# Kernel tuning notes

Measured on AMD Instinct MI355X. Metric: run time of the kernel, lower is better.

The kernel has to match this reference:

```python
import jax, jax.numpy as jnp
import numpy as np

N_NODES = 100_000
N_EDGES = 1_600_000
F_IN, H, C = 128, 128, 64


def setup_inputs() -> dict:
    key = jax.random.key(0)
    ks = jax.random.split(key, 12)
    s = 0.05  # weight init scale
    features = jax.random.normal(ks[0], (N_NODES, F_IN), jnp.float32)
    src = jax.random.randint(ks[1], (N_EDGES,), 0, N_NODES)
    dst = jax.random.randint(ks[2], (N_EDGES,), 0, N_NODES)
    return {
        "features": features,
        "src": src,
        "dst": dst,
        "Ws0": jax.random.normal(ks[3], (F_IN, H), jnp.float32) * s,
        "Wn0": jax.random.normal(ks[4], (F_IN, H), jnp.float32) * s,
        "b0": jnp.zeros((H,), jnp.float32),
        "Ws1": jax.random.normal(ks[5], (H, H), jnp.float32) * s,
        "Wn1": jax.random.normal(ks[6], (H, H), jnp.float32) * s,
        "b1": jnp.zeros((H,), jnp.float32),
        "Ws2": jax.random.normal(ks[7], (H, C), jnp.float32) * s,
        "Wn2": jax.random.normal(ks[8], (H, C), jnp.float32) * s,
        "b2": jnp.zeros((C,), jnp.float32),
    }


def sage_conv(feat, src, dst, Ws, Wn, b):
    """DGL SAGEConv with mean aggregator: fc_self(h) + fc_neigh(mean_{u->v} h_u) + b."""
    n = feat.shape[0]
    deg = jax.ops.segment_sum(jnp.ones(src.shape[0], feat.dtype), dst, num_segments=n)
    # gather src features along edges, reduce by dst (irregular gather-scatter)
    neigh = jax.ops.segment_sum(feat[src], dst, num_segments=n)
    neigh = neigh / jnp.maximum(deg, 1.0)[:, None]
    return feat @ Ws + neigh @ Wn + b


def reference(features, src, dst, Ws0, Wn0, b0, Ws1, Wn1, b1, Ws2, Wn2, b2):
    # eval mode: dropout is identity
    h = sage_conv(features, src, dst, Ws0, Wn0, b0)
    h = jax.nn.relu(h)
    h = sage_conv(h, src, dst, Ws1, Wn1, b1)
    h = jax.nn.relu(h)
    h = sage_conv(h, src, dst, Ws2, Wn2, b2)
    return h
```

## Files before the change

kernel.cpp:

```cpp
#include <hip/hip_runtime.h>

typedef _Float16 f16x8 __attribute__((ext_vector_type(8)));
typedef _Float16 f16x4 __attribute__((ext_vector_type(4)));
typedef _Float16 f16x2 __attribute__((ext_vector_type(2)));
typedef float f32x4 __attribute__((ext_vector_type(4)));


#define BSHIFT 7
#define BSZ 128
#define EPB 16384

__global__ __launch_bounds__(256) void histA(const int* __restrict__ dst,
                                             int* __restrict__ hist_pb,
                                             int n_edges, int nbk) {
  __shared__ unsigned lh[1024];
  for (int i = threadIdx.x; i < nbk; i += 256) lh[i] = 0;
  __syncthreads();
  int base = blockIdx.x * EPB;
  for (int i = threadIdx.x; i < EPB; i += 256) {
    int e = base + i;
    if (e < n_edges) atomicAdd(&lh[dst[e] >> BSHIFT], 1u);
  }
  __syncthreads();
  for (int i = threadIdx.x; i < nbk; i += 256)
    hist_pb[(size_t)blockIdx.x * nbk + i] = (int)lh[i];
}

__global__ __launch_bounds__(256) void sumB1(const int* __restrict__ hist_pb,
                                             int* __restrict__ btot, int nblk, int nbk) {
  int b = blockIdx.x * 256 + threadIdx.x;
  if (b >= nbk) return;
  int s = 0;
  for (int k = 0; k < nblk; ++k) s += hist_pb[(size_t)k * nbk + b];
  btot[b] = s;
}

__global__ __launch_bounds__(1024) void scanB2(const int* __restrict__ btot,
                                               int* __restrict__ bbase, int nbk) {
  __shared__ int buf[1024];
  int t = threadIdx.x;
  int v = (t < nbk) ? btot[t] : 0;
  int x = v;
  buf[t] = x;
  __syncthreads();
#pragma unroll
  for (int off = 1; off < 1024; off <<= 1) {
    int tm = (t >= off) ? buf[t - off] : 0;
    __syncthreads();
    x += tm;
    buf[t] = x;
    __syncthreads();
  }
  if (t < nbk) bbase[t] = x - v;
  if (t == nbk - 1) bbase[nbk] = x;
}

__global__ __launch_bounds__(256) void offsB3(int* __restrict__ hist_pb,
                                              const int* __restrict__ bbase,
                                              int nblk, int nbk) {
  int b = blockIdx.x * 256 + threadIdx.x;
  if (b >= nbk) return;
  int run = bbase[b];
  for (int k = 0; k < nblk; ++k) {
    int t = hist_pb[(size_t)k * nbk + b];
    hist_pb[(size_t)k * nbk + b] = run;
    run += t;
  }
}

__global__ __launch_bounds__(256) void scatC(const int* __restrict__ src,
                                             const int* __restrict__ dst,
                                             const int* __restrict__ hist_pb,
                                             unsigned* __restrict__ pairs,
                                             int n_edges, int nbk) {
  __shared__ unsigned lofs[1024];
  for (int i = threadIdx.x; i < nbk; i += 256)
    lofs[i] = (unsigned)hist_pb[(size_t)blockIdx.x * nbk + i];
  __syncthreads();
  int base = blockIdx.x * EPB;
  for (int i = threadIdx.x; i < EPB; i += 256) {
    int e = base + i;
    if (e < n_edges) {
      int d = dst[e];
      unsigned pos = atomicAdd(&lofs[d >> BSHIFT], 1u);
      pairs[pos] = ((unsigned)(d & (BSZ - 1)) << 18) | (unsigned)src[e];
    }
  }
}

__global__ __launch_bounds__(256) void finalD(const unsigned* __restrict__ pairs,
                                              const int* __restrict__ bbase,
                                              int* __restrict__ deg,
                                              int* __restrict__ row_ptr,
                                              int* __restrict__ src_sorted,
                                              int n, int nbk) {
  __shared__ int ldeg[BSZ];
  __shared__ int lscan[BSZ];
  __shared__ int lcur[BSZ];
  int b = blockIdx.x;
  int t = threadIdx.x;
  int node0 = b << BSHIFT;
  int beg = bbase[b], end = bbase[b + 1];
  if (t < BSZ) ldeg[t] = 0;
  __syncthreads();
  for (int i = beg + t; i < end; i += 256) atomicAdd(&ldeg[pairs[i] >> 18], 1);
  __syncthreads();
  int x = (t < BSZ) ? ldeg[t] : 0;
  if (t < BSZ) lscan[t] = x;
  __syncthreads();
#pragma unroll
  for (int off = 1; off < BSZ; off <<= 1) {
    int tm = (t >= off && t < BSZ) ? lscan[t - off] : 0;
    __syncthreads();
    if (t < BSZ) {
      x += tm;
      lscan[t] = x;
    }
    __syncthreads();
  }
  if (t < BSZ) {
    int node = node0 + t;
    lcur[t] = beg + lscan[t] - ldeg[t];
    if (node < n) {
      deg[node] = ldeg[t];
      row_ptr[node + 1] = beg + lscan[t];
      if (node == 0) row_ptr[0] = 0;
    }
  }
  __syncthreads();
  for (int i = beg + t; i < end; i += 256) {
    unsigned p = pairs[i];
    int pos = atomicAdd(&lcur[p >> 18], 1);
    src_sorted[pos] = (int)(p & 0x3FFFFu);
  }
}

__global__ __launch_bounds__(256) void convert_features(const float* __restrict__ f,
                                                        _Float16* __restrict__ X, int n) {
  int idx = blockIdx.x * 256 + threadIdx.x;
  int total = n * 32;
  if (idx >= total) return;
  int node = idx >> 5;
  int c4 = (idx & 31) * 4;
  float4 v = *(const float4*)(f + (size_t)node * 128 + c4);
  _Float16* o = X + (size_t)node * 256 + c4;
  o[0] = (_Float16)v.x;
  o[1] = (_Float16)v.y;
  o[2] = (_Float16)v.z;
  o[3] = (_Float16)v.w;
}

__global__ __launch_bounds__(256) void build_wt(const float* __restrict__ Ws,
                                                const float* __restrict__ Wn,
                                                _Float16* __restrict__ Wt, int NOUT) {
  int idx = blockIdx.x * 256 + threadIdx.x;
  if (idx >= NOUT * 256) return;
  int nn = idx >> 8;
  int k = idx & 255;
  float v = (k < 128) ? Ws[(size_t)k * NOUT + nn] : Wn[(size_t)(k - 128) * NOUT + nn];
  Wt[(size_t)nn * 256 + k] = (_Float16)v;
}

__global__ __launch_bounds__(256) void aggregate_f16(
    const _Float16* __restrict__ X, const int* __restrict__ row_ptr,
    const int* __restrict__ src_sorted, const int* __restrict__ deg,
    _Float16* __restrict__ Xout, int n) {
  int gid = blockIdx.x * 256 + threadIdx.x;
  int node = gid >> 6;
  if (node >= n) return;
  int lane = threadIdx.x & 63;
  int fh = lane & 31;
  int es = lane >> 5;
  int beg = row_ptr[node];
  int end = row_ptr[node + 1];
  float a0 = 0.f, a1 = 0.f, a2 = 0.f, a3 = 0.f;
  int e = beg;
  for (; e + 8 <= end; e += 8) {
    int s0 = src_sorted[e + 0 + es];
    int s1 = src_sorted[e + 2 + es];
    int s2 = src_sorted[e + 4 + es];
    int s3 = src_sorted[e + 6 + es];
    f16x4 v0 = *(const f16x4*)(X + (size_t)s0 * 256 + fh * 4);
    f16x4 v1 = *(const f16x4*)(X + (size_t)s1 * 256 + fh * 4);
    f16x4 v2 = *(const f16x4*)(X + (size_t)s2 * 256 + fh * 4);
    f16x4 v3 = *(const f16x4*)(X + (size_t)s3 * 256 + fh * 4);
    a0 += (float)v0[0] + (float)v1[0] + (float)v2[0] + (float)v3[0];
    a1 += (float)v0[1] + (float)v1[1] + (float)v2[1] + (float)v3[1];
    a2 += (float)v0[2] + (float)v1[2] + (float)v2[2] + (float)v3[2];
    a3 += (float)v0[3] + (float)v1[3] + (float)v2[3] + (float)v3[3];
  }
  for (; e < end; e += 2) {
    if (e + es < end) {
      int s = src_sorted[e + es];
      f16x4 v = *(const f16x4*)(X + (size_t)s * 256 + fh * 4);
      a0 += (float)v[0];
      a1 += (float)v[1];
      a2 += (float)v[2];
      a3 += (float)v[3];
    }
  }
  a0 += __shfl_xor(a0, 32);
  a1 += __shfl_xor(a1, 32);
  a2 += __shfl_xor(a2, 32);
  a3 += __shfl_xor(a3, 32);
  if (es == 0) {
    float inv = 1.0f / fmaxf((float)(end - beg), 1.0f);
    f16x4 o;
    o[0] = (_Float16)(a0 * inv);
    o[1] = (_Float16)(a1 * inv);
    o[2] = (_Float16)(a2 * inv);
    o[3] = (_Float16)(a3 * inv);
    *(f16x4*)(Xout + (size_t)node * 256 + 128 + fh * 4) = o;
  }
}

template <int NOUT, bool RELU, bool FINAL>
__global__ __launch_bounds__(256) void gemm_mfma(
    const _Float16* __restrict__ X, const _Float16* __restrict__ Wt,
    const float* __restrict__ bias, _Float16* __restrict__ outX,
    float* __restrict__ outF, int n) {
  constexpr int CW = NOUT / 2;
  constexpr int CF = CW / 16;
  __shared__ _Float16 Xs[128][72];
  __shared__ _Float16 Wc[NOUT][72];

  int tid = threadIdx.x;
  int lane = tid & 63;
  int wid = tid >> 6;
  int wr = wid >> 1;
  int wc = wid & 1;
  int node0 = blockIdx.x * 128;

  f32x4 acc[4][CF];
#pragma unroll
  for (int i = 0; i < 4; ++i)
#pragma unroll
    for (int j = 0; j < CF; ++j) acc[i][j] = {0.f, 0.f, 0.f, 0.f};

#pragma unroll
  for (int c = 0; c < 4; ++c) {
    int k0 = c * 64;
#pragma unroll
    for (int i = 0; i < 4; ++i) {
      int idx = i * 256 + tid;
      int r = idx >> 3;
      int o = (idx & 7) * 8;
      f16x8 v;
#pragma unroll
      for (int z = 0; z < 8; ++z) v[z] = (_Float16)0.f;
      int node = node0 + r;
      if (node < n) v = *(const f16x8*)(X + (size_t)node * 256 + k0 + o);
      *(f16x8*)&Xs[r][o] = v;
    }
#pragma unroll
    for (int i = 0; i < NOUT / 32; ++i) {
      int idx = i * 256 + tid;
      int r = idx >> 3;
      int o = (idx & 7) * 8;
      *(f16x8*)&Wc[r][o] = *(const f16x8*)(Wt + (size_t)r * 256 + k0 + o);
    }
    __syncthreads();
#pragma unroll
    for (int ks = 0; ks < 2; ++ks) {
      int kk = ks * 32 + (lane >> 4) * 8;
      f16x8 a[4], b[CF];
#pragma unroll
      for (int i = 0; i < 4; ++i)
        a[i] = *(const f16x8*)&Xs[wr * 64 + i * 16 + (lane & 15)][kk];
#pragma unroll
      for (int j = 0; j < CF; ++j)
        b[j] = *(const f16x8*)&Wc[wc * CW + j * 16 + (lane & 15)][kk];
#pragma unroll
      for (int i = 0; i < 4; ++i)
#pragma unroll
        for (int j = 0; j < CF; ++j)
          acc[i][j] = __builtin_amdgcn_mfma_f32_16x16x32_f16(a[i], b[j], acc[i][j], 0, 0, 0);
    }
    __syncthreads();
  }

#pragma unroll
  for (int j = 0; j < CF; ++j) {
    int col = wc * CW + j * 16 + (lane & 15);
    float bv = bias[col];
#pragma unroll
    for (int i = 0; i < 4; ++i) {
#pragma unroll
      for (int q = 0; q < 4; ++q) {
        int row = wr * 64 + i * 16 + (lane >> 4) * 4 + q;
        int node = node0 + row;
        if (node < n) {
          float v = acc[i][j][q] + bv;
          if (RELU) v = fmaxf(v, 0.f);
          if (FINAL)
            outF[(size_t)node * NOUT + col] = v;
          else
            outX[(size_t)node * 256 + col] = (_Float16)v;
        }
      }
    }
  }
}

extern "C" void kernel_launch(void* const* d_in, const int* in_sizes, int n_in,
                              void* d_out, int out_size, void* d_ws, size_t ws_size,
                              hipStream_t stream) {
  const float* features = (const float*)d_in[0];
  const int* src = (const int*)d_in[1];
  const int* dst = (const int*)d_in[2];
  const float* Ws0 = (const float*)d_in[3];
  const float* Wn0 = (const float*)d_in[4];
  const float* b0 = (const float*)d_in[5];
  const float* Ws1 = (const float*)d_in[6];
  const float* Wn1 = (const float*)d_in[7];
  const float* b1 = (const float*)d_in[8];
  const float* Ws2 = (const float*)d_in[9];
  const float* Wn2 = (const float*)d_in[10];
  const float* b2 = (const float*)d_in[11];

  const int n = in_sizes[0] / 128;
  const int n_edges = in_sizes[1];
  const int nbk = (n + BSZ - 1) >> BSHIFT;
  const int nblk = (n_edges + EPB - 1) / EPB;

  char* ws = (char*)d_ws;
  size_t off = 0;
  auto alloc = [&](size_t bytes) -> void* {
    void* p = ws + off;
    off += (bytes + 255) & ~(size_t)255;
    return p;
  };
  int* hist_pb = (int*)alloc((size_t)nblk * nbk * 4);
  int* btot = (int*)alloc((size_t)nbk * 4);
  int* bbase = (int*)alloc(((size_t)nbk + 1) * 4);
  unsigned* pairs = (unsigned*)alloc((size_t)n_edges * 4);
  int* deg = (int*)alloc((size_t)n * 4);
  int* row_ptr = (int*)alloc(((size_t)n + 1) * 4);
  int* src_sorted = (int*)alloc((size_t)n_edges * 4);
  _Float16* XA = (_Float16*)alloc((size_t)n * 256 * 2);
  _Float16* XB = (_Float16*)alloc((size_t)n * 256 * 2);
  _Float16* Wt0 = (_Float16*)alloc((size_t)128 * 256 * 2);
  _Float16* Wt1 = (_Float16*)alloc((size_t)128 * 256 * 2);
  _Float16* Wt2 = (_Float16*)alloc((size_t)64 * 256 * 2);

  int nbkb = (nbk + 255) / 256;
  histA<<<nblk, 256, 0, stream>>>(dst, hist_pb, n_edges, nbk);
  sumB1<<<nbkb, 256, 0, stream>>>(hist_pb, btot, nblk, nbk);
  scanB2<<<1, 1024, 0, stream>>>(btot, bbase, nbk);
  offsB3<<<nbkb, 256, 0, stream>>>(hist_pb, bbase, nblk, nbk);
  scatC<<<nblk, 256, 0, stream>>>(src, dst, hist_pb, pairs, n_edges, nbk);
  finalD<<<nbk, 256, 0, stream>>>(pairs, bbase, deg, row_ptr, src_sorted, n, nbk);

  convert_features<<<(n * 32 + 255) / 256, 256, 0, stream>>>(features, XA, n);
  build_wt<<<(128 * 256 + 255) / 256, 256, 0, stream>>>(Ws0, Wn0, Wt0, 128);
  build_wt<<<(128 * 256 + 255) / 256, 256, 0, stream>>>(Ws1, Wn1, Wt1, 128);
  build_wt<<<(64 * 256 + 255) / 256, 256, 0, stream>>>(Ws2, Wn2, Wt2, 64);

  int agg_blocks = (int)(((size_t)n * 64 + 255) / 256);
  int gemm_blocks = (n + 127) / 128;

  aggregate_f16<<<agg_blocks, 256, 0, stream>>>(XA, row_ptr, src_sorted, deg, XA, n);
  gemm_mfma<128, true, false><<<gemm_blocks, 256, 0, stream>>>(XA, Wt0, b0, XB, nullptr, n);
  aggregate_f16<<<agg_blocks, 256, 0, stream>>>(XB, row_ptr, src_sorted, deg, XB, n);
  gemm_mfma<128, true, false><<<gemm_blocks, 256, 0, stream>>>(XB, Wt1, b1, XA, nullptr, n);
  aggregate_f16<<<agg_blocks, 256, 0, stream>>>(XA, row_ptr, src_sorted, deg, XA, n);
  gemm_mfma<64, false, true><<<gemm_blocks, 256, 0, stream>>>(XA, Wt2, b2, nullptr, (float*)d_out, n);
}
```

Baseline: 538.4 us.

## Reorder final layer to transform before aggregating, shrink sort blocks, use fma_mix accumulation

The last SAGE layer now computes both linear projections first: one GEMM writes the self term plus bias into the output and the neighbour projection (64 wide, fp16) into a scratch buffer. A new 64-wide aggregation kernel then adds the neighbour mean, so the final gather reads 64 features per edge instead of 128. Separately, the edge-bucketing kernels use smaller edge chunks with a block-to-chunk remap to spread work across XCDs, and the aggregation inner loops use v_fma_mix to accumulate fp16 into fp32 without separate converts. The unused degree array is dropped. Costs: an extra kernel launch, a read-modify-write of the fp32 output, and a larger per-chunk histogram array to sum and scan.

```diff
diff --git a/kernel.cpp b/kernel.cpp
--- a/kernel.cpp
+++ b/kernel.cpp
@@ -2,28 +2,43 @@
 
 typedef _Float16 f16x8 __attribute__((ext_vector_type(8)));
 typedef _Float16 f16x4 __attribute__((ext_vector_type(4)));
-typedef _Float16 f16x2 __attribute__((ext_vector_type(2)));
 typedef float f32x4 __attribute__((ext_vector_type(4)));
 
 
 #define BSHIFT 7
 #define BSZ 128
-#define EPB 16384
+#define EPB 2048
+
+__device__ __forceinline__ int work_of_block(int b, int nblk) {
+  int q = nblk >> 3, r = nblk & 7;
+  int x = b & 7, i = b >> 3;
+  return (x < r) ? x * (q + 1) + i : r * (q + 1) + (x - r) * q + i;
+}
+
+__device__ __forceinline__ void mixlo(float& a, unsigned v) {
+  asm("v_fma_mix_f32 %0, %1, 1.0, %0 op_sel:[0,0,0] op_sel_hi:[1,0,0]"
+      : "+v"(a) : "v"(v));
+}
+__device__ __forceinline__ void mixhi(float& a, unsigned v) {
+  asm("v_fma_mix_f32 %0, %1, 1.0, %0 op_sel:[1,0,0] op_sel_hi:[1,0,0]"
+      : "+v"(a) : "v"(v));
+}
 
 __global__ __launch_bounds__(256) void histA(const int* __restrict__ dst,
                                              int* __restrict__ hist_pb,
-                                             int n_edges, int nbk) {
+                                             int n_edges, int nbk, int nblk) {
   __shared__ unsigned lh[1024];
   for (int i = threadIdx.x; i < nbk; i += 256) lh[i] = 0;
   __syncthreads();
-  int base = blockIdx.x * EPB;
+  int w = work_of_block(blockIdx.x, nblk);
+  int base = w * EPB;
   for (int i = threadIdx.x; i < EPB; i += 256) {
     int e = base + i;
     if (e < n_edges) atomicAdd(&lh[dst[e] >> BSHIFT], 1u);
   }
   __syncthreads();
   for (int i = threadIdx.x; i < nbk; i += 256)
-    hist_pb[(size_t)blockIdx.x * nbk + i] = (int)lh[i];
+    hist_pb[(size_t)w * nbk + i] = (int)lh[i];
 }
 
 __global__ __launch_bounds__(256) void sumB1(const int* __restrict__ hist_pb,
@@ -72,12 +87,13 @@
                                              const int* __restrict__ dst,
                                              const int* __restrict__ hist_pb,
                                              unsigned* __restrict__ pairs,
-                                             int n_edges, int nbk) {
+                                             int n_edges, int nbk, int nblk) {
   __shared__ unsigned lofs[1024];
+  int w = work_of_block(blockIdx.x, nblk);
   for (int i = threadIdx.x; i < nbk; i += 256)
-    lofs[i] = (unsigned)hist_pb[(size_t)blockIdx.x * nbk + i];
-  __syncthreads();
-  int base = blockIdx.x * EPB;
+    lofs[i] = (unsigned)hist_pb[(size_t)w * nbk + i];
+  __syncthreads();
+  int base = w * EPB;
   for (int i = threadIdx.x; i < EPB; i += 256) {
     int e = base + i;
     if (e < n_edges) {
@@ -90,7 +106,6 @@
 
 __global__ __launch_bounds__(256) void finalD(const unsigned* __restrict__ pairs,
                                               const int* __restrict__ bbase,
-                                              int* __restrict__ deg,
                                               int* __restrict__ row_ptr,
                                               int* __restrict__ src_sorted,
                                               int n, int nbk) {
@@ -122,7 +137,6 @@
     int node = node0 + t;
     lcur[t] = beg + lscan[t] - ldeg[t];
     if (node < n) {
-      deg[node] = ldeg[t];
       row_ptr[node + 1] = beg + lscan[t];
       if (node == 0) row_ptr[0] = 0;
     }
@@ -161,10 +175,20 @@
   Wt[(size_t)nn * 256 + k] = (_Float16)v;
 }
 
+__global__ __launch_bounds__(256) void build_wt2cat(const float* __restrict__ Ws2,
+                                                    const float* __restrict__ Wn2,
+                                                    _Float16* __restrict__ Wt) {
+  int idx = blockIdx.x * 256 + threadIdx.x;
+  if (idx >= 128 * 128) return;
+  int nn = idx >> 7;
+  int k = idx & 127;
+  float v = (nn < 64) ? Ws2[(size_t)k * 64 + nn] : Wn2[(size_t)k * 64 + (nn - 64)];
+  Wt[(size_t)nn * 128 + k] = (_Float16)v;
+}
+
 __global__ __launch_bounds__(256) void aggregate_f16(
     const _Float16* __restrict__ X, const int* __restrict__ row_ptr,
-    const int* __restrict__ src_sorted, const int* __restrict__ deg,
-    _Float16* __restrict__ Xout, int n) {
+    const int* __restrict__ src_sorted, _Float16* __restrict__ Xout, int n) {
   int gid = blockIdx.x * 256 + threadIdx.x;
   int node = gid >> 6;
   if (node >= n) return;
@@ -180,23 +204,20 @@
     int s1 = src_sorted[e + 2 + es];
     int s2 = src_sorted[e + 4 + es];
     int s3 = src_sorted[e + 6 + es];
-    f16x4 v0 = *(const f16x4*)(X + (size_t)s0 * 256 + fh * 4);
-    f16x4 v1 = *(const f16x4*)(X + (size_t)s1 * 256 + fh * 4);
-    f16x4 v2 = *(const f16x4*)(X + (size_t)s2 * 256 + fh * 4);
-    f16x4 v3 = *(const f16x4*)(X + (size_t)s3 * 256 + fh * 4);
-    a0 += (float)v0[0] + (float)v1[0] + (float)v2[0] + (float)v3[0];
-    a1 += (float)v0[1] + (float)v1[1] + (float)v2[1] + (float)v3[1];
-    a2 += (float)v0[2] + (float)v1[2] + (float)v2[2] + (float)v3[2];
-    a3 += (float)v0[3] + (float)v1[3] + (float)v2[3] + (float)v3[3];
+    uint2 v0 = *(const uint2*)(X + (size_t)s0 * 256 + fh * 4);
+    uint2 v1 = *(const uint2*)(X + (size_t)s1 * 256 + fh * 4);
+    uint2 v2 = *(const uint2*)(X + (size_t)s2 * 256 + fh * 4);
+    uint2 v3 = *(const uint2*)(X + (size_t)s3 * 256 + fh * 4);
+    mixlo(a0, v0.x); mixhi(a1, v0.x); mixlo(a2, v0.y); mixhi(a3, v0.y);
+    mixlo(a0, v1.x); mixhi(a1, v1.x); mixlo(a2, v1.y); mixhi(a3, v1.y);
+    mixlo(a0, v2.x); mixhi(a1, v2.x); mixlo(a2, v2.y); mixhi(a3, v2.y);
+    mixlo(a0, v3.x); mixhi(a1, v3.x); mixlo(a2, v3.y); mixhi(a3, v3.y);
   }
   for (; e < end; e += 2) {
     if (e + es < end) {
       int s = src_sorted[e + es];
-      f16x4 v = *(const f16x4*)(X + (size_t)s * 256 + fh * 4);
-      a0 += (float)v[0];
-      a1 += (float)v[1];
-      a2 += (float)v[2];
-      a3 += (float)v[3];
+      uint2 v = *(const uint2*)(X + (size_t)s * 256 + fh * 4);
+      mixlo(a0, v.x); mixhi(a1, v.x); mixlo(a2, v.y); mixhi(a3, v.y);
     }
   }
   a0 += __shfl_xor(a0, 32);
@@ -214,11 +235,60 @@
   }
 }
 
-template <int NOUT, bool RELU, bool FINAL>
+__global__ __launch_bounds__(256) void aggregate64_add(
+    const _Float16* __restrict__ T, const int* __restrict__ row_ptr,
+    const int* __restrict__ src_sorted, float* __restrict__ out, int n) {
+  int gid = blockIdx.x * 256 + threadIdx.x;
+  int node = gid >> 6;
+  if (node >= n) return;
+  int lane = threadIdx.x & 63;
+  int fq = lane & 15;
+  int es = lane >> 4;
+  int beg = row_ptr[node];
+  int end = row_ptr[node + 1];
+  float a0 = 0.f, a1 = 0.f, a2 = 0.f, a3 = 0.f;
+  int e = beg;
+  for (; e + 16 <= end; e += 16) {
+    int s0 = src_sorted[e + 0 + es];
+    int s1 = src_sorted[e + 4 + es];
+    int s2 = src_sorted[e + 8 + es];
+    int s3 = src_sorted[e + 12 + es];
+    uint2 v0 = *(const uint2*)(T + (size_t)s0 * 64 + fq * 4);
+    uint2 v1 = *(const uint2*)(T + (size_t)s1 * 64 + fq * 4);
+    uint2 v2 = *(const uint2*)(T + (size_t)s2 * 64 + fq * 4);
+    uint2 v3 = *(const uint2*)(T + (size_t)s3 * 64 + fq * 4);
+    mixlo(a0, v0.x); mixhi(a1, v0.x); mixlo(a2, v0.y); mixhi(a3, v0.y);
+    mixlo(a0, v1.x); mixhi(a1, v1.x); mixlo(a2, v1.y); mixhi(a3, v1.y);
+    mixlo(a0, v2.x); mixhi(a1, v2.x); mixlo(a2, v2.y); mixhi(a3, v2.y);
+    mixlo(a0, v3.x); mixhi(a1, v3.x); mixlo(a2, v3.y); mixhi(a3, v3.y);
+  }
+  for (; e < end; e += 4) {
+    if (e + es < end) {
+      int s = src_sorted[e + es];
+      uint2 v = *(const uint2*)(T + (size_t)s * 64 + fq * 4);
+      mixlo(a0, v.x); mixhi(a1, v.x); mixlo(a2, v.y); mixhi(a3, v.y);
+    }
+  }
+  a0 += __shfl_xor(a0, 16); a0 += __shfl_xor(a0, 32);
+  a1 += __shfl_xor(a1, 16); a1 += __shfl_xor(a1, 32);
+  a2 += __shfl_xor(a2, 16); a2 += __shfl_xor(a2, 32);
+  a3 += __shfl_xor(a3, 16); a3 += __shfl_xor(a3, 32);
+  if (es == 0) {
+    float inv = 1.0f / fmaxf((float)(end - beg), 1.0f);
+    float4* po = (float4*)(out + (size_t)node * 64 + fq * 4);
+    float4 cur = *po;
+    cur.x += a0 * inv;
+    cur.y += a1 * inv;
+    cur.z += a2 * inv;
+    cur.w += a3 * inv;
+    *po = cur;
+  }
+}
+
+template <int NOUT, bool RELU>
 __global__ __launch_bounds__(256) void gemm_mfma(
     const _Float16* __restrict__ X, const _Float16* __restrict__ Wt,
-    const float* __restrict__ bias, _Float16* __restrict__ outX,
-    float* __restrict__ outF, int n) {
+    const float* __restrict__ bias, _Float16* __restrict__ outX, int n) {
   constexpr int CW = NOUT / 2;
   constexpr int CF = CW / 16;
   __shared__ _Float16 Xs[128][72];
@@ -292,10 +362,92 @@
         if (node < n) {
           float v = acc[i][j][q] + bv;
           if (RELU) v = fmaxf(v, 0.f);
-          if (FINAL)
-            outF[(size_t)node * NOUT + col] = v;
+          outX[(size_t)node * 256 + col] = (_Float16)v;
+        }
+      }
+    }
+  }
+}
+
+__global__ __launch_bounds__(256) void gemm_final(
+    const _Float16* __restrict__ X, const _Float16* __restrict__ Wt,
+    const float* __restrict__ b2, float* __restrict__ outF,
+    _Float16* __restrict__ T, int n) {
+  __shared__ _Float16 Xs[128][72];
+  __shared__ _Float16 Wc[128][72];
+
+  int tid = threadIdx.x;
+  int lane = tid & 63;
+  int wid = tid >> 6;
+  int wr = wid >> 1;
+  int wc = wid & 1;
+  int node0 = blockIdx.x * 128;
+
+  f32x4 acc[4][4];
+#pragma unroll
+  for (int i = 0; i < 4; ++i)
+#pragma unroll
+    for (int j = 0; j < 4; ++j) acc[i][j] = {0.f, 0.f, 0.f, 0.f};
+
+#pragma unroll
+  for (int c = 0; c < 2; ++c) {
+    int k0 = c * 64;
+#pragma unroll
+    for (int i = 0; i < 4; ++i) {
+      int idx = i * 256 + tid;
+      int r = idx >> 3;
+      int o = (idx & 7) * 8;
+      f16x8 v;
+#pragma unroll
+      for (int z = 0; z < 8; ++z) v[z] = (_Float16)0.f;
+      int node = node0 + r;
+      if (node < n) v = *(const f16x8*)(X + (size_t)node * 256 + k0 + o);
+      *(f16x8*)&Xs[r][o] = v;
+    }
+#pragma unroll
+    for (int i = 0; i < 4; ++i) {
+      int idx = i * 256 + tid;
+      int r = idx >> 3;
+      int o = (idx & 7) * 8;
+      *(f16x8*)&Wc[r][o] = *(const f16x8*)(Wt + (size_t)r * 128 + k0 + o);
+    }
+    __syncthreads();
+#pragma unroll
+    for (int ks = 0; ks < 2; ++ks) {
+      int kk = ks * 32 + (lane >> 4) * 8;
+      f16x8 a[4], b[4];
+#pragma unroll
+      for (int i = 0; i < 4; ++i)
+        a[i] = *(const f16x8*)&Xs[wr * 64 + i * 16 + (lane & 15)][kk];
+#pragma unroll
+      for (int j = 0; j < 4; ++j)
+        b[j] = *(const f16x8*)&Wc[wc * 64 + j * 16 + (lane & 15)][kk];
+#pragma unroll
+      for (int i = 0; i < 4; ++i)
+#pragma unroll
+        for (int j = 0; j < 4; ++j)
+          acc[i][j] = __builtin_amdgcn_mfma_f32_16x16x32_f16(a[i], b[j], acc[i][j], 0, 0, 0);
+    }
+    __syncthreads();
+  }
+
+#pragma unroll
+  for (int j = 0; j < 4; ++j) {
+    int col = wc * 64 + j * 16 + (lane & 15);
+    bool left = col < 64;
+    float bv = left ? b2[col] : 0.f;
+#pragma unroll
+    for (int i = 0; i < 4; ++i) {
+#pragma unroll
+      for (int q = 0; q < 4; ++q) {
+        int row = wr * 64 + i * 16 + (lane >> 4) * 4 + q;
+        int node = node0 + row;
+        if (node < n) {
+          float v = acc[i][j][q] + bv;
+          if (left)
+            outF[(size_t)node * 64 + col] = v;
           else
-            outX[(size_t)node * 256 + col] = (_Float16)v;
+            T[(size_t)node * 64 + (col - 64)] = (_Float16)v;
         }
       }
     }
@@ -334,35 +486,35 @@
   int* btot = (int*)alloc((size_t)nbk * 4);
   int* bbase = (int*)alloc(((size_t)nbk + 1) * 4);
   unsigned* pairs = (unsigned*)alloc((size_t)n_edges * 4);
-  int* deg = (int*)alloc((size_t)n * 4);
   int* row_ptr = (int*)alloc(((size_t)n + 1) * 4);
   int* src_sorted = (int*)alloc((size_t)n_edges * 4);
   _Float16* XA = (_Float16*)alloc((size_t)n * 256 * 2);
   _Float16* XB = (_Float16*)alloc((size_t)n * 256 * 2);
+  _Float16* T = (_Float16*)alloc((size_t)n * 64 * 2);
   _Float16* Wt0 = (_Float16*)alloc((size_t)128 * 256 * 2);
   _Float16* Wt1 = (_Float16*)alloc((size_t)128 * 256 * 2);
-  _Float16* Wt2 = (_Float16*)alloc((size_t)64 * 256 * 2);
+  _Float16* Wt2 = (_Float16*)alloc((size_t)128 * 128 * 2);
 
   int nbkb = (nbk + 255) / 256;
-  histA<<<nblk, 256, 0, stream>>>(dst, hist_pb, n_edges, nbk);
+  histA<<<nblk, 256, 0, stream>>>(dst, hist_pb, n_edges, nbk, nblk);
   sumB1<<<nbkb, 256, 0, stream>>>(hist_pb, btot, nblk, nbk);
   scanB2<<<1, 1024, 0, stream>>>(btot, bbase, nbk);
   offsB3<<<nbkb, 256, 0, stream>>>(hist_pb, bbase, nblk, nbk);
-  scatC<<<nblk, 256, 0, stream>>>(src, dst, hist_pb, pairs, n_edges, nbk);
-  finalD<<<nbk, 256, 0, stream>>>(pairs, bbase, deg, row_ptr, src_sorted, n, nbk);
+  scatC<<<nblk, 256, 0, stream>>>(src, dst, hist_pb, pairs, n_edges, nbk, nblk);
+  finalD<<<nbk, 256, 0, stream>>>(pairs, bbase, row_ptr, src_sorted, n, nbk);
 
   convert_features<<<(n * 32 + 255) / 256, 256, 0, stream>>>(features, XA, n);
   build_wt<<<(128 * 256 + 255) / 256, 256, 0, stream>>>(Ws0, Wn0, Wt0, 128);
   build_wt<<<(128 * 256 + 255) / 256, 256, 0, stream>>>(Ws1, Wn1, Wt1, 128);
-  build_wt<<<(64 * 256 + 255) / 256, 256, 0, stream>>>(Ws2, Wn2, Wt2, 64);
+  build_wt2cat<<<(128 * 128 + 255) / 256, 256, 0, stream>>>(Ws2, Wn2, Wt2);
 
   int agg_blocks = (int)(((size_t)n * 64 + 255) / 256);
   int gemm_blocks = (n + 127) / 128;
 
-  aggregate_f16<<<agg_blocks, 256, 0, stream>>>(XA, row_ptr, src_sorted, deg, XA, n);
-  gemm_mfma<128, true, false><<<gemm_blocks, 256, 0, stream>>>(XA, Wt0, b0, XB, nullptr, n);
-  aggregate_f16<<<agg_blocks, 256, 0, stream>>>(XB, row_ptr, src_sorted, deg, XB, n);
-  gemm_mfma<128, true, false><<<gemm_blocks, 256, 0, stream>>>(XB, Wt1, b1, XA, nullptr, n);
-  aggregate_f16<<<agg_blocks, 256, 0, stream>>>(XA, row_ptr, src_sorted, deg, XA, n);
-  gemm_mfma<64, false, true><<<gemm_blocks, 256, 0, stream>>>(XA, Wt2, b2, nullptr, (float*)d_out, n);
-}
+  aggregate_f16<<<agg_blocks, 256, 0, stream>>>(XA, row_ptr, src_sorted, XA, n);
+  gemm_mfma<128, true><<<gemm_blocks, 256, 0, stream>>>(XA, Wt0, b0, XB, n);
+  aggregate_f16<<<agg_blocks, 256, 0, stream>>>(XB, row_ptr, src_sorted, XB, n);
+  gemm_mfma<128, true><<<gemm_blocks, 256, 0, stream>>>(XB, Wt1, b1, XA, n);
+  gemm_final<<<gemm_blocks, 256, 0, stream>>>(XA, Wt2, b2, (float*)d_out, T, n);
+  aggregate64_add<<<agg_blocks, 256, 0, stream>>>(T, row_ptr, src_sorted, (float*)d_out, n);
+}
```

Measured after the change: 710.6 us. 1.32x slower.
